# Kernel optimization log

Hardware: AMD Instinct MI355X
Metric: run time of the kernel (lower is better)

## Reference

```python
import jax, jax.numpy as jnp
import numpy as np

EPS = 1e-5  # BatchNorm eps (torch default)


def setup_inputs() -> dict:
    B, C, H, W = 8, 256, 128, 128
    Cr = C // 4
    key = jax.random.key(0)
    ks = jax.random.split(key, 12)
    s = lambda *sh: 1.0 / np.sqrt(np.prod(sh[1:]) if len(sh) > 1 else sh[0])
    return {
        "x": jax.random.normal(ks[0], (B, C, H, W), jnp.float32),
        "text_feat": jax.random.normal(ks[1], (B, C), jnp.float32),
        # spatial_proj: Conv2d(C,C,1) + BatchNorm2d(C) (eval-mode running stats)
        "proj_w": jax.random.normal(ks[2], (C, C), jnp.float32) * s(C, C),
        "proj_b": jax.random.normal(ks[3], (C,), jnp.float32) * 0.02,
        "bn_gamma": jnp.ones((C,), jnp.float32),
        "bn_beta": jnp.zeros((C,), jnp.float32),
        "bn_mean": jnp.zeros((C,), jnp.float32),
        "bn_var": jnp.ones((C,), jnp.float32),
        # channel_attention: Conv2d(C,C/4,1) -> ReLU -> Conv2d(C/4,C,1) -> Sigmoid
        "ca_w1": jax.random.normal(ks[4], (Cr, C), jnp.float32) * s(Cr, C),
        "ca_b1": jax.random.normal(ks[5], (Cr,), jnp.float32) * 0.02,
        "ca_w2": jax.random.normal(ks[6], (C, Cr), jnp.float32) * s(C, Cr),
        "ca_b2": jax.random.normal(ks[7], (C,), jnp.float32) * 0.02,
        # spatial_attention: Conv2d(2,1,7,padding=3) -> Sigmoid
        "sa_w": jax.random.normal(ks[8], (1, 2, 7, 7), jnp.float32) * s(1, 2 * 49),
        "sa_b": jax.random.normal(ks[9], (1,), jnp.float32) * 0.02,
    }


def _forward(x, text_feat, proj_w, proj_b, bn_gamma, bn_beta, bn_mean, bn_var,
             ca_w1, ca_b1, ca_w2, ca_b2, sa_w, sa_b):
    B, C, H, W = x.shape
    # spatial_proj on the spatially-constant broadcast of text_feat: 1x1 conv + BN
    # + ReLU are pointwise, so compute once per (B,C) vector and broadcast.
    t = jnp.einsum('oc,bc->bo', proj_w, text_feat) + proj_b          # (B,C)
    t = (t - bn_mean) * (bn_gamma / jnp.sqrt(bn_var + EPS)) + bn_beta
    t = jax.nn.relu(t)                                               # (B,C)
    # channel attention: global-avg-pool of a constant map is the value itself
    h = jax.nn.relu(jnp.einsum('rc,bc->br', ca_w1, t) + ca_b1)       # (B,C/4)
    channel_weight = jax.nn.sigmoid(jnp.einsum('cr,br->bc', ca_w2, h) + ca_b2)  # (B,C)
    # spatial attention: channel mean/max are per-batch constants, but the 7x7
    # zero-padded conv has edge effects, so run the real conv on broadcast maps.
    avg_feat = jnp.mean(t, axis=1)                                   # (B,)
    max_feat = jnp.max(t, axis=1)                                    # (B,)
    am = jnp.broadcast_to(jnp.stack([avg_feat, max_feat], axis=1)[:, :, None, None],
                          (B, 2, H, W))                              # (B,2,H,W)
    sw = jax.lax.conv_general_dilated(
        am, sa_w, window_strides=(1, 1), padding=((3, 3), (3, 3)),
        dimension_numbers=('NCHW', 'OIHW', 'NCHW')) + sa_b[None, :, None, None]
    spatial_weight = jax.nn.sigmoid(sw)                              # (B,1,H,W)
    return x * channel_weight[:, :, None, None] * spatial_weight


def reference(x, text_feat, proj_w, proj_b, bn_gamma, bn_beta, bn_mean, bn_var,
              ca_w1, ca_b1, ca_w2, ca_b2, sa_w, sa_b):
    return _forward(x, text_feat, proj_w, proj_b, bn_gamma, bn_beta, bn_mean,
                    bn_var, ca_w1, ca_b1, ca_w2, ca_b2, sa_w, sa_b)
```

## Files before the change

kernel.cpp:

```cpp
#include <hip/hip_runtime.h>
#include <math.h>

#define B 8
#define C 256
#define CR 64
#define H 128
#define W 128
#define HW (H*W)
#define NELEM (B*C*HW)
#define N4 (NELEM/4)

typedef float floatx4 __attribute__((ext_vector_type(4)));

__device__ __forceinline__ float sigmoidf_(float z) {
    return 1.0f / (1.0f + expf(-z));
}

__global__ __launch_bounds__(256)
void setup_kernel(const float* __restrict__ tf,
                  const float* __restrict__ pw,
                  const float* __restrict__ pb,
                  const float* __restrict__ g,
                  const float* __restrict__ be,
                  const float* __restrict__ mu,
                  const float* __restrict__ var,
                  const float* __restrict__ w1,
                  const float* __restrict__ b1,
                  const float* __restrict__ w2,
                  const float* __restrict__ b2,
                  const float* __restrict__ saw,
                  const float* __restrict__ sab,
                  float* __restrict__ cw,
                  float* __restrict__ swm)
{
    const int b   = blockIdx.x;
    const int tid = threadIdx.x;

    __shared__ float tf_sh[C];
    __shared__ float t_sh[C];
    __shared__ float h_sh[CR];
    __shared__ float red[8];
    __shared__ float s_stats[2];
    __shared__ float saw_sh[98];
    __shared__ float table[49];

    tf_sh[tid] = tf[b * C + tid];
    if (tid < 98) saw_sh[tid] = saw[tid];
    __syncthreads();

    float acc = 0.0f;
    {
        const float4* pwr = reinterpret_cast<const float4*>(pw + tid * C);
        #pragma unroll 8
        for (int k4 = 0; k4 < C / 4; ++k4) {
            const float4 wv = pwr[k4];
            const float* tfk = &tf_sh[k4 * 4];
            acc += wv.x * tfk[0] + wv.y * tfk[1] + wv.z * tfk[2] + wv.w * tfk[3];
        }
    }
    float t;
    {
        const float scale = g[tid] * rsqrtf(var[tid] + 1e-5f);
        t = (acc + pb[tid] - mu[tid]) * scale + be[tid];
        t = fmaxf(t, 0.0f);
        t_sh[tid] = t;
    }

    {
        float s = t, m = t;
        #pragma unroll
        for (int off = 32; off > 0; off >>= 1) {
            s += __shfl_down(s, off);
            m  = fmaxf(m, __shfl_down(m, off));
        }
        const int wv_ = tid >> 6;
        if ((tid & 63) == 0) { red[wv_] = s; red[4 + wv_] = m; }
        __syncthreads();
        if (tid == 0) {
            s_stats[0] = (red[0] + red[1] + red[2] + red[3]) * (1.0f / C);
            s_stats[1] = fmaxf(fmaxf(red[4], red[5]), fmaxf(red[6], red[7]));
        }
        __syncthreads();
    }

    if (tid < 49) {
        const int yc = tid / 7, xc = tid % 7;
        const int ky0 = yc < 3 ? 3 - yc : 0;
        const int ky1 = yc > 3 ? 9 - yc : 6;
        const int kx0 = xc < 3 ? 3 - xc : 0;
        const int kx1 = xc > 3 ? 9 - xc : 6;
        float S0 = 0.0f, S1 = 0.0f;
        for (int ky = ky0; ky <= ky1; ++ky)
            for (int kx = kx0; kx <= kx1; ++kx) {
                S0 += saw_sh[ky * 7 + kx];
                S1 += saw_sh[49 + ky * 7 + kx];
            }
        table[tid] = sigmoidf_(s_stats[0] * S0 + s_stats[1] * S1 + sab[0]);
    }

    if (tid < CR) {
        float a = b1[tid];
        const float4* w1r = reinterpret_cast<const float4*>(w1 + tid * C);
        #pragma unroll 8
        for (int k4 = 0; k4 < C / 4; ++k4) {
            const float4 wv = w1r[k4];
            const float* tk = &t_sh[k4 * 4];
            a += wv.x * tk[0] + wv.y * tk[1] + wv.z * tk[2] + wv.w * tk[3];
        }
        h_sh[tid] = fmaxf(a, 0.0f);
    }
    __syncthreads();

    {
        float a = b2[tid];
        const float4* w2r = reinterpret_cast<const float4*>(w2 + tid * CR);
        #pragma unroll
        for (int r4 = 0; r4 < CR / 4; ++r4) {
            const float4 wv = w2r[r4];
            const float* hk = &h_sh[r4 * 4];
            a += wv.x * hk[0] + wv.y * hk[1] + wv.z * hk[2] + wv.w * hk[3];
        }
        cw[b * C + tid] = sigmoidf_(a);
    }

    for (int s_ = tid; s_ < HW; s_ += 256) {
        const int y = s_ >> 7;
        const int x = s_ & (W - 1);
        const int yc = y < 3 ? y : (y > 124 ? y - 121 : 3);
        const int xc = x < 3 ? x : (x > 124 ? x - 121 : 3);
        swm[b * HW + s_] = table[yc * 7 + xc];
    }
}

__global__ __launch_bounds__(256)
void fuse_kernel(const floatx4* __restrict__ x4,
                 const float*   __restrict__ cw,
                 const float4*  __restrict__ sw4,
                 floatx4* __restrict__ out4)
{
    const int stride = gridDim.x * blockDim.x;
    for (int j = blockIdx.x * blockDim.x + threadIdx.x; j < N4; j += stride) {
        const int s4 = j & 4095;
        const int c  = (j >> 12) & 255;
        const int b  = j >> 20;
        const float cwv = cw[(b << 8) + c];
        const floatx4 xs = __builtin_nontemporal_load(&x4[j]);
        const float4 sws = sw4[(b << 12) + s4];
        floatx4 o;
        o.x = xs.x * cwv * sws.x;
        o.y = xs.y * cwv * sws.y;
        o.z = xs.z * cwv * sws.z;
        o.w = xs.w * cwv * sws.w;
        __builtin_nontemporal_store(o, &out4[j]);
    }
}

extern "C" void kernel_launch(void* const* d_in, const int* in_sizes, int n_in,
                              void* d_out, int out_size, void* d_ws, size_t ws_size,
                              hipStream_t stream) {
    const float* x    = (const float*)d_in[0];
    const float* tf   = (const float*)d_in[1];
    const float* pw   = (const float*)d_in[2];
    const float* pb   = (const float*)d_in[3];
    const float* g    = (const float*)d_in[4];
    const float* be   = (const float*)d_in[5];
    const float* mu   = (const float*)d_in[6];
    const float* var  = (const float*)d_in[7];
    const float* w1   = (const float*)d_in[8];
    const float* b1   = (const float*)d_in[9];
    const float* w2   = (const float*)d_in[10];
    const float* b2   = (const float*)d_in[11];
    const float* saw  = (const float*)d_in[12];
    const float* sab  = (const float*)d_in[13];
    float* out = (float*)d_out;

    float* wsf   = (float*)d_ws;
    float* cw    = wsf;
    float* swm   = wsf + 2048;

    setup_kernel<<<B, 256, 0, stream>>>(tf, pw, pb, g, be, mu, var,
                                        w1, b1, w2, b2, saw, sab, cw, swm);
    fuse_kernel<<<2048, 256, 0, stream>>>((const floatx4*)x, cw,
                                          (const float4*)swm, (floatx4*)out);
}
```

Measured before the change: 69.94 us.

## Replace materialized spatial-weight map with 7x7 lookup table in fused kernel

The setup kernel stops writing a full per-batch HxW spatial-weight map and instead emits only the 49-entry edge-case sigmoid table per batch. The fuse kernel stages channel weights and these tables in shared memory and reconstructs the spatial weight from row and column position, removing the per-element global load of the spatial map. This cuts setup kernel store traffic and fuse kernel read traffic, at the cost of a prologue copy and a sync in every fuse block plus some branching. Unroll factors of the setup dot products are also raised.

```diff
diff --git a/kernel.cpp b/kernel.cpp
--- a/kernel.cpp
+++ b/kernel.cpp
@@ -31,7 +31,7 @@
                   const float* __restrict__ saw,
                   const float* __restrict__ sab,
                   float* __restrict__ cw,
-                  float* __restrict__ swm)
+                  float* __restrict__ tbl)
 {
     const int b   = blockIdx.x;
     const int tid = threadIdx.x;
@@ -42,7 +42,6 @@
     __shared__ float red[8];
     __shared__ float s_stats[2];
     __shared__ float saw_sh[98];
-    __shared__ float table[49];
 
     tf_sh[tid] = tf[b * C + tid];
     if (tid < 98) saw_sh[tid] = saw[tid];
@@ -51,7 +50,7 @@
     float acc = 0.0f;
     {
         const float4* pwr = reinterpret_cast<const float4*>(pw + tid * C);
-        #pragma unroll 8
+        #pragma unroll 16
         for (int k4 = 0; k4 < C / 4; ++k4) {
             const float4 wv = pwr[k4];
             const float* tfk = &tf_sh[k4 * 4];
@@ -95,13 +94,13 @@
                 S0 += saw_sh[ky * 7 + kx];
                 S1 += saw_sh[49 + ky * 7 + kx];
             }
-        table[tid] = sigmoidf_(s_stats[0] * S0 + s_stats[1] * S1 + sab[0]);
+        tbl[b * 49 + tid] = sigmoidf_(s_stats[0] * S0 + s_stats[1] * S1 + sab[0]);
     }
 
     if (tid < CR) {
         float a = b1[tid];
         const float4* w1r = reinterpret_cast<const float4*>(w1 + tid * C);
-        #pragma unroll 8
+        #pragma unroll 16
         for (int k4 = 0; k4 < C / 4; ++k4) {
             const float4 wv = w1r[k4];
             const float* tk = &t_sh[k4 * 4];
@@ -122,35 +121,49 @@
         }
         cw[b * C + tid] = sigmoidf_(a);
     }
-
-    for (int s_ = tid; s_ < HW; s_ += 256) {
-        const int y = s_ >> 7;
-        const int x = s_ & (W - 1);
-        const int yc = y < 3 ? y : (y > 124 ? y - 121 : 3);
-        const int xc = x < 3 ? x : (x > 124 ? x - 121 : 3);
-        swm[b * HW + s_] = table[yc * 7 + xc];
-    }
 }
 
 __global__ __launch_bounds__(256)
 void fuse_kernel(const floatx4* __restrict__ x4,
                  const float*   __restrict__ cw,
-                 const float4*  __restrict__ sw4,
+                 const float*   __restrict__ tbl,
                  floatx4* __restrict__ out4)
 {
+    __shared__ float cw_sh[B * C];
+    __shared__ float tbl_sh[B * 49];
+
+    const int tid = threadIdx.x;
+    {
+        const float4* cwsrc = reinterpret_cast<const float4*>(cw);
+        float4* cwdst = reinterpret_cast<float4*>(cw_sh);
+        #pragma unroll
+        for (int i = tid; i < (B * C) / 4; i += 256) cwdst[i] = cwsrc[i];
+        for (int i = tid; i < B * 49; i += 256) tbl_sh[i] = tbl[i];
+    }
+    __syncthreads();
+
     const int stride = gridDim.x * blockDim.x;
-    for (int j = blockIdx.x * blockDim.x + threadIdx.x; j < N4; j += stride) {
+    for (int j = blockIdx.x * blockDim.x + tid; j < N4; j += stride) {
         const int s4 = j & 4095;
-        const int c  = (j >> 12) & 255;
-        const int b  = j >> 20;
-        const float cwv = cw[(b << 8) + c];
+        const int bc = j >> 12;
+        const int b  = bc >> 8;
+        const int y  = s4 >> 5;
+        const int xg = s4 & 31;
+        const int yc = y < 3 ? y : (y > 124 ? y - 121 : 3);
+
+        const float cwv = cw_sh[bc];
+        const float* tb = &tbl_sh[b * 49 + yc * 7];
+        float s0, s1, s2, s3;
+        if (xg == 0)       { s0 = tb[0]; s1 = tb[1]; s2 = tb[2]; s3 = tb[3]; }
+        else if (xg == 31) { s0 = tb[3]; s1 = tb[4]; s2 = tb[5]; s3 = tb[6]; }
+        else               { s0 = s1 = s2 = s3 = tb[3]; }
+
         const floatx4 xs = __builtin_nontemporal_load(&x4[j]);
-        const float4 sws = sw4[(b << 12) + s4];
         floatx4 o;
-        o.x = xs.x * cwv * sws.x;
-        o.y = xs.y * cwv * sws.y;
-        o.z = xs.z * cwv * sws.z;
-        o.w = xs.w * cwv * sws.w;
+        o.x = xs.x * cwv * s0;
+        o.y = xs.y * cwv * s1;
+        o.z = xs.z * cwv * s2;
+        o.w = xs.w * cwv * s3;
         __builtin_nontemporal_store(o, &out4[j]);
     }
 }
@@ -174,12 +187,12 @@
     const float* sab  = (const float*)d_in[13];
     float* out = (float*)d_out;
 
-    float* wsf   = (float*)d_ws;
-    float* cw    = wsf;
-    float* swm   = wsf + 2048;
+    float* wsf = (float*)d_ws;
+    float* cw  = wsf;
+    float* tbl = wsf + 2048;
 
     setup_kernel<<<B, 256, 0, stream>>>(tf, pw, pb, g, be, mu, var,
-                                        w1, b1, w2, b2, saw, sab, cw, swm);
-    fuse_kernel<<<2048, 256, 0, stream>>>((const floatx4*)x, cw,
-                                          (const float4*)swm, (floatx4*)out);
+                                        w1, b1, w2, b2, saw, sab, cw, tbl);
+    fuse_kernel<<<2048, 256, 0, stream>>>((const floatx4*)x, cw, tbl,
+                                          (floatx4*)out);
 }
```

New measurement: 69.08 us. About the same (-1.2%).
